# Performance work log

Measured on AMD Instinct MI355X. Metric: run time of the kernel, lower is better.

Reference implementation:

```python
import jax, jax.numpy as jnp
import numpy as np

N_HEAD = 12
D_HEAD = 64


def setup_inputs() -> dict:
    key = jax.random.key(0)
    ks = jax.random.split(key, 9)
    bs, seq, d_model = 4, 2048, 768
    sc = 1.0 / np.sqrt(d_model)
    return {
        "q": jax.random.normal(ks[0], (bs, seq, d_model), jnp.float32),
        "k": jax.random.normal(ks[1], (bs, seq, d_model), jnp.float32),
        "v": jax.random.normal(ks[2], (bs, seq, d_model), jnp.float32),
        "Wq": jax.random.normal(ks[3], (d_model, d_model), jnp.float32) * sc,
        "bq": jax.random.normal(ks[4], (d_model,), jnp.float32) * 0.01,
        "Wk": jax.random.normal(ks[5], (d_model, d_model), jnp.float32) * sc,
        "bk": jax.random.normal(ks[6], (d_model,), jnp.float32) * 0.01,
        "Wv": jax.random.normal(ks[7], (d_model, d_model), jnp.float32) * sc,
        "bv": jax.random.normal(ks[8], (d_model,), jnp.float32) * 0.01,
    }


def _split_heads(x):
    # [bs, seq, n_head*d_head] -> [bs, n_head, seq, d_head]
    bs, seq, _ = x.shape
    return x.reshape(bs, seq, N_HEAD, D_HEAD).transpose(0, 2, 1, 3)


def reference(q, k, v, Wq, bq, Wk, bk, Wv, bv):
    # Linear projections (torch Linear: x @ W.T + b)
    wq = _split_heads(q @ Wq.T + bq)
    wk = _split_heads(k @ Wk.T + bk)
    wv = _split_heads(v @ Wv.T + bv)
    # scale=False in defaults -> raw dot products, no mask, dropout is eval no-op
    scores = jnp.einsum("bhqd,bhkd->bhqk", wq, wk)  # [bs, h, S, S]
    probs = jax.nn.softmax(scores, axis=-1)
    attn_vec = jnp.einsum("bhqk,bhkd->bhqd", probs, wv)
    bs, _, seq, _ = attn_vec.shape
    # merge heads -> [bs, seq, n_head*d_head]
    return attn_vec.transpose(0, 2, 1, 3).reshape(bs, seq, N_HEAD * D_HEAD)
```

## Files before the change

kernel.cpp:

```cpp
#include <hip/hip_runtime.h>
#include <stdint.h>

typedef _Float16 half8  __attribute__((ext_vector_type(8)));
typedef _Float16 half4v __attribute__((ext_vector_type(4)));
typedef float    floatx4 __attribute__((ext_vector_type(4)));

#define LOG2E 1.44269504088896340736f

__device__ __forceinline__ void gl_lds16(const _Float16* g, _Float16* l) {
  __builtin_amdgcn_global_load_lds(
      (__attribute__((address_space(1))) void*)g,
      (__attribute__((address_space(3))) void*)l, 16, 0, 0);
}

__device__ __forceinline__ half4v pack4(float a, float b, float c, float d) {
  auto lo = __builtin_amdgcn_cvt_pkrtz(a, b);
  auto hi = __builtin_amdgcn_cvt_pkrtz(c, d);
  return half4v{static_cast<_Float16>(lo[0]), static_cast<_Float16>(lo[1]),
                static_cast<_Float16>(hi[0]), static_cast<_Float16>(hi[1])};
}

struct CvtArgs {
  const float* src[3];
  _Float16*    dst[3];
};

__global__ void cvt_kernel(CvtArgs a) {
  const int z = blockIdx.y;
  const int i = (blockIdx.x * 256 + threadIdx.x) * 8;
  const float4* s = (const float4*)(a.src[z] + i);
  float4 v0 = s[0], v1 = s[1];
  half8 h = { (_Float16)v0.x, (_Float16)v0.y, (_Float16)v0.z, (_Float16)v0.w,
              (_Float16)v1.x, (_Float16)v1.y, (_Float16)v1.z, (_Float16)v1.w };
  *(half8*)(a.dst[z] + i) = h;
}


__device__ __forceinline__ void gemm_stage16(const _Float16* __restrict__ P,
                                             _Float16* sb, int r0, int k0, int tid) {
  #pragma unroll
  for (int i = 0; i < 2; ++i) {
    int G = i * 256 + tid;
    int r = G >> 2, gl = G & 3;
    int g = gl ^ ((r >> 1) & 3);
    gl_lds16(P + (size_t)(r0 + r) * 768 + k0 + g * 8, sb + G * 8);
  }
}

__device__ __forceinline__ void gemm_issueA(const float* __restrict__ X,
                                            int m0, int k0, int tid,
                                            float4& a0, float4& a1,
                                            float4& b0, float4& b1) {
  {
    int G = tid;
    int r = G >> 2, gl = G & 3;
    int g = gl ^ ((r >> 1) & 3);
    const float4* s = (const float4*)(X + (size_t)(m0 + r) * 768 + k0 + g * 8);
    a0 = s[0]; a1 = s[1];
  }
  {
    int G = 256 + tid;
    int r = G >> 2, gl = G & 3;
    int g = gl ^ ((r >> 1) & 3);
    const float4* s = (const float4*)(X + (size_t)(m0 + r) * 768 + k0 + g * 8);
    b0 = s[0]; b1 = s[1];
  }
}

__device__ __forceinline__ void gemm_writeA(_Float16* Asb, int tid,
                                            const float4& a0, const float4& a1,
                                            const float4& b0, const float4& b1) {
  half8 h0 = { (_Float16)a0.x, (_Float16)a0.y, (_Float16)a0.z, (_Float16)a0.w,
               (_Float16)a1.x, (_Float16)a1.y, (_Float16)a1.z, (_Float16)a1.w };
  *(half8*)(Asb + tid * 8) = h0;
  half8 h1 = { (_Float16)b0.x, (_Float16)b0.y, (_Float16)b0.z, (_Float16)b0.w,
               (_Float16)b1.x, (_Float16)b1.y, (_Float16)b1.z, (_Float16)b1.w };
  *(half8*)(Asb + (256 + tid) * 8) = h1;
}

template <int BUF>
__device__ __forceinline__ void gemm_body(
    int knext, const float* __restrict__ X, const _Float16* __restrict__ W,
    _Float16* As, _Float16* Bs, int m0, int n0, int tid, int z,
    int wr, int wc, int qd, int col, floatx4 (&acc)[4][4])
{
  const bool pref = (knext < 768);
  float4 a0, a1, b0, b1;
  if (pref) {
    gemm_issueA(X, m0, knext, tid, a0, a1, b0, b1);
    gemm_stage16(W, Bs + (1 - BUF) * 4096, n0, knext, tid);
  }

  half8 af[4], bf[4];
  #pragma unroll
  for (int t = 0; t < 4; ++t) {
    int ra = wr * 64 + t * 16 + col;
    af[t] = *(const half8*)(As + BUF * 4096 + ra * 32 + ((qd ^ ((ra >> 1) & 3)) * 8));
  }
  #pragma unroll
  for (int t = 0; t < 4; ++t) {
    int rb = wc * 64 + t * 16 + col;
    bf[t] = *(const half8*)(Bs + BUF * 4096 + rb * 32 + ((qd ^ ((rb >> 1) & 3)) * 8));
  }
  if (z == 2) {
    #pragma unroll
    for (int i = 0; i < 4; ++i)
      #pragma unroll
      for (int j = 0; j < 4; ++j)
        acc[i][j] = __builtin_amdgcn_mfma_f32_16x16x32_f16(af[i], bf[j], acc[i][j], 0, 0, 0);
  } else {
    #pragma unroll
    for (int i = 0; i < 4; ++i)
      #pragma unroll
      for (int j = 0; j < 4; ++j)
        acc[i][j] = __builtin_amdgcn_mfma_f32_16x16x32_f16(bf[j], af[i], acc[i][j], 0, 0, 0);
  }

  if (pref)
    gemm_writeA(As + (1 - BUF) * 4096, tid, a0, a1, b0, b1);
  __syncthreads();
}

__global__ __launch_bounds__(256, 2) void qkv_gemm(
    const float* __restrict__ qx, const float* __restrict__ kx, const float* __restrict__ vx,
    const _Float16* __restrict__ wh,
    const float* __restrict__ bqp, const float* __restrict__ bkp, const float* __restrict__ bvp,
    _Float16* __restrict__ oq, _Float16* __restrict__ ok, _Float16* __restrict__ ovt)
{
  __shared__ __attribute__((aligned(16))) char smem[40960];
  _Float16* As = (_Float16*)smem;
  _Float16* Bs = (_Float16*)(smem + 16384);
  _Float16* Es = (_Float16*)smem;

  const int z  = blockIdx.z;
  const float* X = (z == 0) ? qx : ((z == 1) ? kx : vx);
  const _Float16* W = wh + (size_t)z * 589824;
  const int m0 = blockIdx.x * 128, n0 = blockIdx.y * 128;
  const int tid  = threadIdx.x;
  const int lane = tid & 63, wid = tid >> 6;
  const int wr = wid >> 1, wc = wid & 1;
  const int qd = lane >> 4, col = lane & 15;

  const floatx4 z4 = {0.f, 0.f, 0.f, 0.f};
  floatx4 acc[4][4];
  #pragma unroll
  for (int i = 0; i < 4; ++i)
    #pragma unroll
    for (int j = 0; j < 4; ++j) acc[i][j] = z4;

  {
    float4 a0, a1, b0, b1;
    gemm_issueA(X, m0, 0, tid, a0, a1, b0, b1);
    gemm_stage16(W, Bs, n0, 0, tid);
    gemm_writeA(As, tid, a0, a1, b0, b1);
  }
  __syncthreads();
  for (int kk = 0; kk < 768; kk += 64) {
    gemm_body<0>(kk + 32, X, W, As, Bs, m0, n0, tid, z, wr, wc, qd, col, acc);
    gemm_body<1>(kk + 64, X, W, As, Bs, m0, n0, tid, z, wr, wc, qd, col, acc);
  }

  const float* bias = (z == 0) ? bqp : ((z == 1) ? bkp : bvp);
  const int b = m0 >> 11, s0 = m0 & 2047;
  if (z == 2) {
    #pragma unroll
    for (int j = 0; j < 4; ++j) {
      int n_loc = wc * 64 + j * 16 + col;
      float bb = bias[n0 + n_loc];
      #pragma unroll
      for (int i = 0; i < 4; ++i) {
        int s_loc = wr * 64 + i * 16 + qd * 4;
        half4v h = pack4(acc[i][j][0] + bb, acc[i][j][1] + bb,
                         acc[i][j][2] + bb, acc[i][j][3] + bb);
        *(half4v*)(Es + n_loc * 160 + s_loc) = h;
      }
    }
    __syncthreads();
    #pragma unroll
    for (int it = 0; it < 8; ++it) {
      int row = it * 16 + (tid >> 4);
      int k   = tid & 15;
      half8 vr = *(const half8*)(Es + row * 160 + k * 8);
      *(half8*)(ovt + ((size_t)(b * 768 + n0 + row)) * 2048 + s0 + k * 8) = vr;
    }
  } else {
    _Float16* O = (z == 0) ? oq : ok;
    const float scale = (z == 0) ? LOG2E : 1.0f;
    #pragma unroll
    for (int j = 0; j < 4; ++j) {
      int n_loc = wc * 64 + j * 16 + qd * 4;
      float4 bb = *(const float4*)(bias + n0 + n_loc);
      #pragma unroll
      for (int i = 0; i < 4; ++i) {
        int s_loc = wr * 64 + i * 16 + col;
        half4v h = pack4((acc[i][j][0] + bb.x) * scale, (acc[i][j][1] + bb.y) * scale,
                         (acc[i][j][2] + bb.z) * scale, (acc[i][j][3] + bb.w) * scale);
        *(half4v*)(Es + s_loc * 160 + n_loc) = h;
      }
    }
    __syncthreads();
    const int hh0 = n0 >> 6;
    #pragma unroll
    for (int it = 0; it < 8; ++it) {
      int seg = it * 32 + (tid >> 3);
      int s = seg >> 1, hseg = seg & 1;
      int k = tid & 7;
      half8 vr = *(const half8*)(Es + s * 160 + hseg * 64 + k * 8);
      int mb = (m0 + s) >> 11, sg = (m0 + s) & 2047;
      *(half8*)(O + (size_t)(mb * 12 + hh0 + hseg) * 131072
                  + (size_t)sg * 64 + k * 8) = vr;
    }
  }
}


__device__ __forceinline__ void stage_kv(const _Float16* __restrict__ Kg,
                                         const _Float16* __restrict__ Vg,
                                         _Float16* ksd, _Float16* vsd, int j0, int tid) {
  #pragma unroll
  for (int i = 0; i < 2; ++i) {
    int c = i * 256 + tid;
    int row = c >> 3, sc = c & 7;
    gl_lds16(Kg + (size_t)(j0 + row) * 64 + ((sc ^ (row & 7)) * 8), ksd + c * 8);
    gl_lds16(Vg + (size_t)row * 2048 + j0 + ((sc ^ (row & 7)) * 8), vsd + c * 8);
  }
}

template <int BUF>
__device__ __forceinline__ void attn_body(
    int jnext, const _Float16* __restrict__ Kg, const _Float16* __restrict__ Vg,
    _Float16* Ks, _Float16* Vs, int tid,
    const half8 (&qf)[2][2], int kb0, int kb1, const int (&vb)[4],
    floatx4 (&negm)[2], floatx4 (&ol)[2], floatx4 (&o)[4][2])
{
  if (jnext < 2048)
    stage_kv(Kg, Vg, Ks + (1 - BUF) * 4096, Vs + (1 - BUF) * 4096, jnext, tid);

  const char* ksb = (const char*)Ks;
  const char* vsb = (const char*)Vs;

  floatx4 st[4][2];
  #pragma unroll
  for (int t = 0; t < 4; ++t) {
    half8 kf0 = *(const half8*)(ksb + BUF * 8192 + t * 2048 + kb0);
    half8 kf1 = *(const half8*)(ksb + BUF * 8192 + t * 2048 + kb1);
    #pragma unroll
    for (int qt = 0; qt < 2; ++qt) {
      st[t][qt] = __builtin_amdgcn_mfma_f32_16x16x32_f16(kf0, qf[qt][0], negm[qt], 0, 0, 0);
      st[t][qt] = __builtin_amdgcn_mfma_f32_16x16x32_f16(kf1, qf[qt][1], st[t][qt], 0, 0, 0);
    }
  }

  float mr[2];
  #pragma unroll
  for (int qt = 0; qt < 2; ++qt) {
    float v = fmaxf(
        fmaxf(fmaxf(fmaxf(st[0][qt][0], st[0][qt][1]), fmaxf(st[0][qt][2], st[0][qt][3])),
              fmaxf(fmaxf(st[1][qt][0], st[1][qt][1]), fmaxf(st[1][qt][2], st[1][qt][3]))),
        fmaxf(fmaxf(fmaxf(st[2][qt][0], st[2][qt][1]), fmaxf(st[2][qt][2], st[2][qt][3])),
              fmaxf(fmaxf(st[3][qt][0], st[3][qt][1]), fmaxf(st[3][qt][2], st[3][qt][3]))));
    v = fmaxf(v, __shfl_xor(v, 16, 64));
    v = fmaxf(v, __shfl_xor(v, 32, 64));
    mr[qt] = fmaxf(v, 0.f);
  }

  half4v pf[4][2];
  #pragma unroll
  for (int qt = 0; qt < 2; ++qt)
    #pragma unroll
    for (int t = 0; t < 4; ++t)
      pf[t][qt] = pack4(__builtin_amdgcn_exp2f(st[t][qt][0] - mr[qt]),
                        __builtin_amdgcn_exp2f(st[t][qt][1] - mr[qt]),
                        __builtin_amdgcn_exp2f(st[t][qt][2] - mr[qt]),
                        __builtin_amdgcn_exp2f(st[t][qt][3] - mr[qt]));

  if (__any(mr[0] > 0.f || mr[1] > 0.f)) {
    #pragma unroll
    for (int qt = 0; qt < 2; ++qt) {
      float al = __builtin_amdgcn_exp2f(-mr[qt]);
      negm[qt] -= mr[qt];
      ol[qt] *= al;
      #pragma unroll
      for (int dt = 0; dt < 4; ++dt) o[dt][qt] *= al;
    }
  }

  const half4v vone = {(_Float16)1.0f, (_Float16)1.0f, (_Float16)1.0f, (_Float16)1.0f};
  #pragma unroll
  for (int dt = 0; dt < 4; ++dt) {
    #pragma unroll
    for (int t = 0; t < 4; ++t) {
      half4v vf = *(const half4v*)(vsb + BUF * 8192 + dt * 2048 + vb[t]);
      #pragma unroll
      for (int qt = 0; qt < 2; ++qt)
        o[dt][qt] = __builtin_amdgcn_mfma_f32_16x16x16f16(vf, pf[t][qt], o[dt][qt], 0, 0, 0);
    }
  }
  #pragma unroll
  for (int t = 0; t < 4; ++t)
    #pragma unroll
    for (int qt = 0; qt < 2; ++qt)
      ol[qt] = __builtin_amdgcn_mfma_f32_16x16x16f16(vone, pf[t][qt], ol[qt], 0, 0, 0);

  __syncthreads();
}

__global__ __launch_bounds__(256, 3) void attn_kernel(
    const _Float16* __restrict__ Qm,
    const _Float16* __restrict__ Km,
    const _Float16* __restrict__ Vt,
    float* __restrict__ out)
{
  __shared__ __attribute__((aligned(16))) _Float16 Ks[2 * 4096];
  __shared__ __attribute__((aligned(16))) _Float16 Vs[2 * 4096];
  const int bh = blockIdx.x;
  const int q0 = blockIdx.y * 128;
  const int tid = threadIdx.x, lane = tid & 63, w = tid >> 6;
  const int qd = lane >> 4, col = lane & 15, c7 = col & 7;
  const _Float16* Qg = Qm + (size_t)bh * 131072;
  const _Float16* Kg = Km + (size_t)bh * 131072;
  const _Float16* Vg = Vt + (size_t)bh * 131072;

  half8 qf[2][2];
  #pragma unroll
  for (int qt = 0; qt < 2; ++qt)
    #pragma unroll
    for (int ks = 0; ks < 2; ++ks)
      qf[qt][ks] = *(const half8*)(Qg + (size_t)(q0 + w * 32 + qt * 16 + col) * 64
                                   + (ks * 4 + qd) * 8);

  const int kb0 = col * 128 + ((qd ^ c7) * 16);
  const int kb1 = col * 128 + (((4 + qd) ^ c7) * 16);
  const int vq = (qd >> 1) ^ c7;
  int vb[4];
  #pragma unroll
  for (int t = 0; t < 4; ++t)
    vb[t] = col * 128 + (qd & 1) * 8 + ((vq ^ (2 * t)) * 16);

  floatx4 negm[2] = {{100.f, 100.f, 100.f, 100.f}, {100.f, 100.f, 100.f, 100.f}};
  const floatx4 z4 = {0.f, 0.f, 0.f, 0.f};
  floatx4 ol[2] = {z4, z4};
  floatx4 o[4][2];
  #pragma unroll
  for (int dt = 0; dt < 4; ++dt)
    #pragma unroll
    for (int qt = 0; qt < 2; ++qt) o[dt][qt] = z4;

  stage_kv(Kg, Vg, Ks, Vs, 0, tid);
  __syncthreads();

  for (int jj = 0; jj < 2048; jj += 128) {
    attn_body<0>(jj + 64,  Kg, Vg, Ks, Vs, tid, qf, kb0, kb1, vb, negm, ol, o);
    attn_body<1>(jj + 128, Kg, Vg, Ks, Vs, tid, qf, kb0, kb1, vb, negm, ol, o);
  }

  const int b = bh / 12, h = bh % 12;
  #pragma unroll
  for (int qt = 0; qt < 2; ++qt) {
    float inv = 1.0f / ol[qt][0];
    int qg = q0 + w * 32 + qt * 16 + col;
    float* obase = out + ((size_t)b * 2048 + qg) * 768 + h * 64;
    #pragma unroll
    for (int dt = 0; dt < 4; ++dt) {
      floatx4 v = o[dt][qt];
      v *= inv;
      *(floatx4*)(obase + dt * 16 + qd * 4) = v;
    }
  }
}

extern "C" void kernel_launch(void* const* d_in, const int* in_sizes, int n_in,
                              void* d_out, int out_size, void* d_ws, size_t ws_size,
                              hipStream_t stream) {
  const float* q  = (const float*)d_in[0];
  const float* k  = (const float*)d_in[1];
  const float* v  = (const float*)d_in[2];
  const float* Wq = (const float*)d_in[3];
  const float* bq = (const float*)d_in[4];
  const float* Wk = (const float*)d_in[5];
  const float* bk = (const float*)d_in[6];
  const float* Wv = (const float*)d_in[7];
  const float* bv = (const float*)d_in[8];

  const size_t NX = 6291456;
  const size_t NW = 589824;
  const size_t need = (3 * NW + 3 * NX) * sizeof(_Float16);
  if (ws_size < need) return;

  _Float16* wh = (_Float16*)d_ws;
  _Float16* qh = wh + 3 * NW;
  _Float16* kh = qh + NX;
  _Float16* vt = kh + NX;

  CvtArgs ca;
  ca.src[0] = Wq; ca.src[1] = Wk; ca.src[2] = Wv;
  ca.dst[0] = wh; ca.dst[1] = wh + NW; ca.dst[2] = wh + 2 * NW;

  cvt_kernel<<<dim3(288, 3), 256, 0, stream>>>(ca);
  qkv_gemm<<<dim3(64, 6, 3), 256, 0, stream>>>(q, k, v, wh, bq, bk, bv, qh, kh, vt);
  attn_kernel<<<dim3(48, 16), 256, 0, stream>>>(qh, kh, vt, (float*)d_out);
}
```

Measured before the change: 266.5 us.

## Fuse weight fp16 conversion into QKV GEMM and use persistent tile loop

Removes the separate kernel that converted the three weight matrices to fp16, and instead loads fp32 weights directly in the GEMM and converts them in registers before writing them to LDS, just as the activations already were. The GEMM grid becomes a persistent 512-block launch that loops over the 1152 output tiles. This saves a launch and a workspace round trip, but the weight tiles are now re-read as fp32 by every tile, which doubles their global traffic and adds register pressure. The tile loop also leaves an uneven tail of work across blocks.

```diff
diff --git a/kernel.cpp b/kernel.cpp
--- a/kernel.cpp
+++ b/kernel.cpp
@@ -20,75 +20,49 @@
                 static_cast<_Float16>(hi[0]), static_cast<_Float16>(hi[1])};
 }
 
-struct CvtArgs {
-  const float* src[3];
-  _Float16*    dst[3];
-};
-
-__global__ void cvt_kernel(CvtArgs a) {
-  const int z = blockIdx.y;
-  const int i = (blockIdx.x * 256 + threadIdx.x) * 8;
-  const float4* s = (const float4*)(a.src[z] + i);
-  float4 v0 = s[0], v1 = s[1];
-  half8 h = { (_Float16)v0.x, (_Float16)v0.y, (_Float16)v0.z, (_Float16)v0.w,
-              (_Float16)v1.x, (_Float16)v1.y, (_Float16)v1.z, (_Float16)v1.w };
-  *(half8*)(a.dst[z] + i) = h;
-}
-
-
-__device__ __forceinline__ void gemm_stage16(const _Float16* __restrict__ P,
-                                             _Float16* sb, int r0, int k0, int tid) {
-  #pragma unroll
-  for (int i = 0; i < 2; ++i) {
-    int G = i * 256 + tid;
-    int r = G >> 2, gl = G & 3;
-    int g = gl ^ ((r >> 1) & 3);
-    gl_lds16(P + (size_t)(r0 + r) * 768 + k0 + g * 8, sb + G * 8);
-  }
-}
-
-__device__ __forceinline__ void gemm_issueA(const float* __restrict__ X,
-                                            int m0, int k0, int tid,
+
+__device__ __forceinline__ void issue_panel(const float* __restrict__ P,
+                                            int r0, int k0, int tid,
                                             float4& a0, float4& a1,
                                             float4& b0, float4& b1) {
   {
     int G = tid;
     int r = G >> 2, gl = G & 3;
     int g = gl ^ ((r >> 1) & 3);
-    const float4* s = (const float4*)(X + (size_t)(m0 + r) * 768 + k0 + g * 8);
+    const float4* s = (const float4*)(P + (size_t)(r0 + r) * 768 + k0 + g * 8);
     a0 = s[0]; a1 = s[1];
   }
   {
     int G = 256 + tid;
     int r = G >> 2, gl = G & 3;
     int g = gl ^ ((r >> 1) & 3);
-    const float4* s = (const float4*)(X + (size_t)(m0 + r) * 768 + k0 + g * 8);
+    const float4* s = (const float4*)(P + (size_t)(r0 + r) * 768 + k0 + g * 8);
     b0 = s[0]; b1 = s[1];
   }
 }
 
-__device__ __forceinline__ void gemm_writeA(_Float16* Asb, int tid,
+__device__ __forceinline__ void write_panel(_Float16* sb, int tid,
                                             const float4& a0, const float4& a1,
                                             const float4& b0, const float4& b1) {
   half8 h0 = { (_Float16)a0.x, (_Float16)a0.y, (_Float16)a0.z, (_Float16)a0.w,
                (_Float16)a1.x, (_Float16)a1.y, (_Float16)a1.z, (_Float16)a1.w };
-  *(half8*)(Asb + tid * 8) = h0;
+  *(half8*)(sb + tid * 8) = h0;
   half8 h1 = { (_Float16)b0.x, (_Float16)b0.y, (_Float16)b0.z, (_Float16)b0.w,
                (_Float16)b1.x, (_Float16)b1.y, (_Float16)b1.z, (_Float16)b1.w };
-  *(half8*)(Asb + (256 + tid) * 8) = h1;
+  *(half8*)(sb + (256 + tid) * 8) = h1;
 }
 
 template <int BUF>
 __device__ __forceinline__ void gemm_body(
-    int knext, const float* __restrict__ X, const _Float16* __restrict__ W,
+    int knext, const float* __restrict__ X, const float* __restrict__ W,
     _Float16* As, _Float16* Bs, int m0, int n0, int tid, int z,
     int wr, int wc, int qd, int col, floatx4 (&acc)[4][4])
 {
   const bool pref = (knext < 768);
-  float4 a0, a1, b0, b1;
+  float4 xa0, xa1, xb0, xb1, wa0, wa1, wb0, wb1;
   if (pref) {
-    gemm_issueA(X, m0, knext, tid, a0, a1, b0, b1);
-    gemm_stage16(W, Bs + (1 - BUF) * 4096, n0, knext, tid);
+    issue_panel(X, m0, knext, tid, xa0, xa1, xb0, xb1);
+    issue_panel(W, n0, knext, tid, wa0, wa1, wb0, wb1);
   }
 
   half8 af[4], bf[4];
@@ -116,14 +90,16 @@
         acc[i][j] = __builtin_amdgcn_mfma_f32_16x16x32_f16(bf[j], af[i], acc[i][j], 0, 0, 0);
   }
 
-  if (pref)
-    gemm_writeA(As + (1 - BUF) * 4096, tid, a0, a1, b0, b1);
+  if (pref) {
+    write_panel(As + (1 - BUF) * 4096, tid, xa0, xa1, xb0, xb1);
+    write_panel(Bs + (1 - BUF) * 4096, tid, wa0, wa1, wb0, wb1);
+  }
   __syncthreads();
 }
 
 __global__ __launch_bounds__(256, 2) void qkv_gemm(
     const float* __restrict__ qx, const float* __restrict__ kx, const float* __restrict__ vx,
-    const _Float16* __restrict__ wh,
+    const float* __restrict__ Wqp, const float* __restrict__ Wkp, const float* __restrict__ Wvp,
     const float* __restrict__ bqp, const float* __restrict__ bkp, const float* __restrict__ bvp,
     _Float16* __restrict__ oq, _Float16* __restrict__ ok, _Float16* __restrict__ ovt)
 {
@@ -132,83 +108,90 @@
   _Float16* Bs = (_Float16*)(smem + 16384);
   _Float16* Es = (_Float16*)smem;
 
-  const int z  = blockIdx.z;
-  const float* X = (z == 0) ? qx : ((z == 1) ? kx : vx);
-  const _Float16* W = wh + (size_t)z * 589824;
-  const int m0 = blockIdx.x * 128, n0 = blockIdx.y * 128;
   const int tid  = threadIdx.x;
   const int lane = tid & 63, wid = tid >> 6;
   const int wr = wid >> 1, wc = wid & 1;
   const int qd = lane >> 4, col = lane & 15;
 
-  const floatx4 z4 = {0.f, 0.f, 0.f, 0.f};
-  floatx4 acc[4][4];
-  #pragma unroll
-  for (int i = 0; i < 4; ++i)
-    #pragma unroll
-    for (int j = 0; j < 4; ++j) acc[i][j] = z4;
-
-  {
-    float4 a0, a1, b0, b1;
-    gemm_issueA(X, m0, 0, tid, a0, a1, b0, b1);
-    gemm_stage16(W, Bs, n0, 0, tid);
-    gemm_writeA(As, tid, a0, a1, b0, b1);
-  }
-  __syncthreads();
-  for (int kk = 0; kk < 768; kk += 64) {
-    gemm_body<0>(kk + 32, X, W, As, Bs, m0, n0, tid, z, wr, wc, qd, col, acc);
-    gemm_body<1>(kk + 64, X, W, As, Bs, m0, n0, tid, z, wr, wc, qd, col, acc);
-  }
-
-  const float* bias = (z == 0) ? bqp : ((z == 1) ? bkp : bvp);
-  const int b = m0 >> 11, s0 = m0 & 2047;
-  if (z == 2) {
-    #pragma unroll
-    for (int j = 0; j < 4; ++j) {
-      int n_loc = wc * 64 + j * 16 + col;
-      float bb = bias[n0 + n_loc];
-      #pragma unroll
-      for (int i = 0; i < 4; ++i) {
-        int s_loc = wr * 64 + i * 16 + qd * 4;
-        half4v h = pack4(acc[i][j][0] + bb, acc[i][j][1] + bb,
-                         acc[i][j][2] + bb, acc[i][j][3] + bb);
-        *(half4v*)(Es + n_loc * 160 + s_loc) = h;
+  #pragma unroll 1
+  for (int t = blockIdx.x; t < 1152; t += 512) {
+    const int m0 = (t & 63) * 128;
+    const int n0 = ((t >> 6) % 6) * 128;
+    const int z  = t / 384;
+    const float* X = (z == 0) ? qx : ((z == 1) ? kx : vx);
+    const float* W = (z == 0) ? Wqp : ((z == 1) ? Wkp : Wvp);
+
+    const floatx4 z4 = {0.f, 0.f, 0.f, 0.f};
+    floatx4 acc[4][4];
+    #pragma unroll
+    for (int i = 0; i < 4; ++i)
+      #pragma unroll
+      for (int j = 0; j < 4; ++j) acc[i][j] = z4;
+
+    {
+      float4 xa0, xa1, xb0, xb1, wa0, wa1, wb0, wb1;
+      issue_panel(X, m0, 0, tid, xa0, xa1, xb0, xb1);
+      issue_panel(W, n0, 0, tid, wa0, wa1, wb0, wb1);
+      __syncthreads();
+      write_panel(As, tid, xa0, xa1, xb0, xb1);
+      write_panel(Bs, tid, wa0, wa1, wb0, wb1);
+    }
+    __syncthreads();
+    for (int kk = 0; kk < 768; kk += 64) {
+      gemm_body<0>(kk + 32, X, W, As, Bs, m0, n0, tid, z, wr, wc, qd, col, acc);
+      gemm_body<1>(kk + 64, X, W, As, Bs, m0, n0, tid, z, wr, wc, qd, col, acc);
+    }
+
+    const float* bias = (z == 0) ? bqp : ((z == 1) ? bkp : bvp);
+    const int b = m0 >> 11, s0 = m0 & 2047;
+    if (z == 2) {
+      #pragma unroll
+      for (int j = 0; j < 4; ++j) {
+        int n_loc = wc * 64 + j * 16 + col;
+        float bb = bias[n0 + n_loc];
+        #pragma unroll
+        for (int i = 0; i < 4; ++i) {
+          int s_loc = wr * 64 + i * 16 + qd * 4;
+          half4v h = pack4(acc[i][j][0] + bb, acc[i][j][1] + bb,
+                           acc[i][j][2] + bb, acc[i][j][3] + bb);
+          *(half4v*)(Es + n_loc * 160 + s_loc) = h;
+        }
       }
-    }
-    __syncthreads();
-    #pragma unroll
-    for (int it = 0; it < 8; ++it) {
-      int row = it * 16 + (tid >> 4);
-      int k   = tid & 15;
-      half8 vr = *(const half8*)(Es + row * 160 + k * 8);
-      *(half8*)(ovt + ((size_t)(b * 768 + n0 + row)) * 2048 + s0 + k * 8) = vr;
-    }
-  } else {
-    _Float16* O = (z == 0) ? oq : ok;
-    const float scale = (z == 0) ? LOG2E : 1.0f;
-    #pragma unroll
-    for (int j = 0; j < 4; ++j) {
-      int n_loc = wc * 64 + j * 16 + qd * 4;
-      float4 bb = *(const float4*)(bias + n0 + n_loc);
-      #pragma unroll
-      for (int i = 0; i < 4; ++i) {
-        int s_loc = wr * 64 + i * 16 + col;
-        half4v h = pack4((acc[i][j][0] + bb.x) * scale, (acc[i][j][1] + bb.y) * scale,
-                         (acc[i][j][2] + bb.z) * scale, (acc[i][j][3] + bb.w) * scale);
-        *(half4v*)(Es + s_loc * 160 + n_loc) = h;
+      __syncthreads();
+      #pragma unroll
+      for (int it = 0; it < 8; ++it) {
+        int row = it * 16 + (tid >> 4);
+        int k   = tid & 15;
+        half8 vr = *(const half8*)(Es + row * 160 + k * 8);
+        *(half8*)(ovt + ((size_t)(b * 768 + n0 + row)) * 2048 + s0 + k * 8) = vr;
       }
-    }
-    __syncthreads();
-    const int hh0 = n0 >> 6;
-    #pragma unroll
-    for (int it = 0; it < 8; ++it) {
-      int seg = it * 32 + (tid >> 3);
-      int s = seg >> 1, hseg = seg & 1;
-      int k = tid & 7;
-      half8 vr = *(const half8*)(Es + s * 160 + hseg * 64 + k * 8);
-      int mb = (m0 + s) >> 11, sg = (m0 + s) & 2047;
-      *(half8*)(O + (size_t)(mb * 12 + hh0 + hseg) * 131072
-                  + (size_t)sg * 64 + k * 8) = vr;
+    } else {
+      _Float16* O = (z == 0) ? oq : ok;
+      const float scale = (z == 0) ? LOG2E : 1.0f;
+      #pragma unroll
+      for (int j = 0; j < 4; ++j) {
+        int n_loc = wc * 64 + j * 16 + qd * 4;
+        float4 bb = *(const float4*)(bias + n0 + n_loc);
+        #pragma unroll
+        for (int i = 0; i < 4; ++i) {
+          int s_loc = wr * 64 + i * 16 + col;
+          half4v h = pack4((acc[i][j][0] + bb.x) * scale, (acc[i][j][1] + bb.y) * scale,
+                           (acc[i][j][2] + bb.z) * scale, (acc[i][j][3] + bb.w) * scale);
+          *(half4v*)(Es + s_loc * 160 + n_loc) = h;
+        }
+      }
+      __syncthreads();
+      const int hh0 = n0 >> 6;
+      #pragma unroll
+      for (int it = 0; it < 8; ++it) {
+        int seg = it * 32 + (tid >> 3);
+        int s = seg >> 1, hseg = seg & 1;
+        int k = tid & 7;
+        half8 vr = *(const half8*)(Es + s * 160 + hseg * 64 + k * 8);
+        int mb = (m0 + s) >> 11, sg = (m0 + s) & 2047;
+        *(half8*)(O + (size_t)(mb * 12 + hh0 + hseg) * 131072
+                    + (size_t)sg * 64 + k * 8) = vr;
+      }
     }
   }
 }
@@ -383,20 +366,13 @@
   const float* bv = (const float*)d_in[8];
 
   const size_t NX = 6291456;
-  const size_t NW = 589824;
-  const size_t need = (3 * NW + 3 * NX) * sizeof(_Float16);
+  const size_t need = 3 * NX * sizeof(_Float16);
   if (ws_size < need) return;
 
-  _Float16* wh = (_Float16*)d_ws;
-  _Float16* qh = wh + 3 * NW;
+  _Float16* qh = (_Float16*)d_ws;
   _Float16* kh = qh + NX;
   _Float16* vt = kh + NX;
 
-  CvtArgs ca;
-  ca.src[0] = Wq; ca.src[1] = Wk; ca.src[2] = Wv;
-  ca.dst[0] = wh; ca.dst[1] = wh + NW; ca.dst[2] = wh + 2 * NW;
-
-  cvt_kernel<<<dim3(288, 3), 256, 0, stream>>>(ca);
-  qkv_gemm<<<dim3(64, 6, 3), 256, 0, stream>>>(q, k, v, wh, bq, bk, bv, qh, kh, vt);
+  qkv_gemm<<<dim3(512), 256, 0, stream>>>(q, k, v, Wq, Wk, Wv, bq, bk, bv, qh, kh, vt);
   attn_kernel<<<dim3(48, 16), 256, 0, stream>>>(qh, kh, vt, (float*)d_out);
 }
```

Result: slower. 273.4 us (+2.6%).
